# Optimization experiments

Measured on AMD Instinct MI355X. Metric: run time of the kernel, lower is better.

The kernel has to match this reference:

```python
import jax, jax.numpy as jnp
import numpy as np

B, N, S, DG, C_IN, C_OUT, HID = 2, 128, 4, 8, 4, 8, 32


def setup_inputs() -> dict:
    key = jax.random.key(0)
    ks = jax.random.split(key, 10)

    def w(k, shape, fan_in):
        return jax.random.normal(k, shape, jnp.float32) / np.float32(np.sqrt(fan_in))

    return {
        "pairwise_g": jax.random.normal(ks[0], (B, N, N, S, S, DG), jnp.float32),
        "coset_functions": jax.random.normal(ks[1], (B, N, S, C_IN), jnp.float32),
        "mask": jax.random.bernoulli(ks[2], 0.9, (B, N, S)),
        "ky_W1": w(ks[3], (C_IN, HID, 2), 2), "ky_b1": jnp.zeros((C_IN, HID), jnp.float32),
        "ky_W2": w(ks[4], (C_IN, HID, HID), HID), "ky_b2": jnp.zeros((C_IN, HID), jnp.float32),
        "ky_W3": w(ks[5], (C_IN, 1, HID), HID), "ky_b3": jnp.zeros((C_IN, 1), jnp.float32),
        "kg_W1": w(ks[6], (C_IN, HID, DG), DG), "kg_b1": jnp.zeros((C_IN, HID), jnp.float32),
        "kg_W2": w(ks[7], (C_IN, HID, HID), HID), "kg_b2": jnp.zeros((C_IN, HID), jnp.float32),
        "kg_W3": w(ks[8], (C_IN, 1, HID), HID), "kg_b3": jnp.zeros((C_IN, 1), jnp.float32),
        "w_out": w(ks[9], (C_OUT, C_IN), C_IN),
    }


def _mlp(x, W1, b1, W2, b2, W3, b3):
    # NerualNetKernel with bn=False, act=Swish: (Linear + SiLU) x 3, incl. output layer.
    h = jax.nn.silu(x @ W1.T + b1)
    h = jax.nn.silu(h @ W2.T + b2)
    return jax.nn.silu(h @ W3.T + b3)


def reference(pairwise_g, coset_functions, mask,
              ky_W1, ky_b1, ky_W2, ky_b2, ky_W3, ky_b3,
              kg_W1, kg_b1, kg_W2, kg_b2, kg_W3, kg_b3, w_out):
    b, n, _, s, _, _ = pairwise_g.shape
    c_in = coset_functions.shape[-1]
    key_mask = mask[:, None, :, None, :, None]  # (B,1,N,1,S,1) masks key points/samples
    outs = []
    for i in range(c_in):  # fixed small channel loop, as in the original module
        f = coset_functions[..., i:i + 1]  # (B,N,S,1)
        y1 = jnp.broadcast_to(f[:, None, :, None, :, :], (b, n, n, s, s, 1))  # key side
        y2 = jnp.broadcast_to(f[:, :, None, :, None, :], (b, n, n, s, s, 1))  # query side
        y = jnp.concatenate([y1, y2], axis=-1)  # (B,N,N,S,S,2)
        k = (_mlp(y, ky_W1[i], ky_b1[i], ky_W2[i], ky_b2[i], ky_W3[i], ky_b3[i])
             + _mlp(pairwise_g, kg_W1[i], kg_b1[i], kg_W2[i], kg_b2[i], kg_W3[i], kg_b3[i]))
        att = jnp.where(key_mask, jnp.exp(k), jnp.zeros((), k.dtype))  # (B,N,N,S,S,1)
        att = att / att.sum(axis=(2, 4), keepdims=True)
        f = f + (att * f[:, None, :, None, :, :]).sum(axis=(2, 4))  # residual + weighted agg
        outs.append(f)
    cf = jnp.concatenate(outs, axis=-1)  # (B,N,S,C_IN)
    cf = cf * mask[..., None].astype(cf.dtype)
    return cf @ w_out.T  # (B,N,S,C_OUT), bias-free output transform
```

## Files before the change

kernel.cpp:

```cpp
#include <hip/hip_runtime.h>
#include <hip/hip_bf16.h>

#define BB   2
#define NN   128
#define SS   4
#define DGG  8
#define CIN  4
#define COUT 8
#define HH   32

typedef __attribute__((ext_vector_type(4))) float          fvec4;
typedef __attribute__((ext_vector_type(4))) unsigned short usvec4;
typedef __attribute__((ext_vector_type(8))) unsigned short usvec8;
typedef __attribute__((ext_vector_type(2))) __fp16         half2v;
typedef __attribute__((ext_vector_type(8))) __fp16         f16x8;
typedef __attribute__((ext_vector_type(4))) float          f32x4;
typedef __attribute__((ext_vector_type(4))) unsigned int   uvec4;

__device__ __forceinline__ float bf2f(unsigned short u) {
    return __uint_as_float(((unsigned int)u) << 16);
}
__device__ __forceinline__ float silu_f(float x) {
    float e = __builtin_amdgcn_exp2f(x * -1.44269504f);
    return x * __builtin_amdgcn_rcpf(1.0f + e);
}
__device__ __forceinline__ float exp_f(float x) {
    return __builtin_amdgcn_exp2f(x * 1.44269504f);
}

__device__ __forceinline__ half2v upk(unsigned int u) {
    union { unsigned int u; half2v h; } x; x.u = u; return x.h;
}
__device__ __forceinline__ unsigned int pk2u(float a, float b) {
#if __has_builtin(__builtin_amdgcn_cvt_pkrtz)
    half2v h = __builtin_amdgcn_cvt_pkrtz(a, b);
#else
    half2v h; h[0] = (__fp16)a; h[1] = (__fp16)b;
#endif
    union { half2v h; unsigned int u; } x; x.h = h; return x.u;
}
union FU { uvec4 u; f16x8 h; };
__device__ __forceinline__ f16x8 mk_frag(unsigned a, unsigned b, unsigned c, unsigned d) {
    FU x; x.u = (uvec4){a, b, c, d}; return x.h;
}

__device__ __forceinline__ float loadS(const void* p, int idx, int fmode) {
    return fmode ? bf2f(((const unsigned short*)p)[idx])
                 : ((const float*)p)[idx];
}
__device__ __forceinline__ void load8(const void* p, int base, int fmode, float* dst) {
    if (fmode) {
        usvec8 v = *(const usvec8*)((const unsigned short*)p + base);
#pragma unroll
        for (int d = 0; d < 8; ++d) dst[d] = bf2f(v[d]);
    } else {
        fvec4 a = *(const fvec4*)((const float*)p + base);
        fvec4 b = *(const fvec4*)((const float*)p + base + 4);
        dst[0] = a[0]; dst[1] = a[1]; dst[2] = a[2]; dst[3] = a[3];
        dst[4] = b[0]; dst[5] = b[1]; dst[6] = b[2]; dst[7] = b[3];
    }
}
__device__ __forceinline__ uvec4 load_row8u(const void* p, int eoff, int fmode) {
    uvec4 u;
    if (fmode) {
        usvec8 v = *(const usvec8*)((const unsigned short*)p + eoff);
#pragma unroll
        for (int q = 0; q < 4; ++q) u[q] = pk2u(bf2f(v[2 * q]), bf2f(v[2 * q + 1]));
    } else {
        fvec4 a = *(const fvec4*)((const float*)p + eoff);
        fvec4 b = *(const fvec4*)((const float*)p + eoff + 4);
        u[0] = pk2u(a[0], a[1]); u[1] = pk2u(a[2], a[3]);
        u[2] = pk2u(b[0], b[1]); u[3] = pk2u(b[2], b[3]);
    }
    return u;
}
__device__ __forceinline__ f16x8 load_row8(const void* p, int eoff, int fmode) {
    uvec4 u = load_row8u(p, eoff, fmode);
    return mk_frag(u[0], u[1], u[2], u[3]);
}
__device__ __forceinline__ int load_mask(const void* p, int idx, int mmode) {
    if (mmode == 0) return ((const int*)p)[idx] != 0;
    if (mmode == 1) return ((const unsigned short*)p)[idx] != 0;
    if (mmode == 2) return ((const unsigned char*)p)[idx] != 0;
    return ((const unsigned int*)p)[idx] != 0;
}
__device__ __forceinline__ void stage_pk(unsigned int* dst, const void* src,
                                         int pairs, int fmode, int tid) {
    if (fmode) {
        const unsigned short* s = (const unsigned short*)src;
        for (int x = tid; x < pairs; x += 256)
            dst[x] = pk2u(bf2f(s[2 * x]), bf2f(s[2 * x + 1]));
    } else {
        const float* s = (const float*)src;
        for (int x = tid; x < pairs; x += 256)
            dst[x] = pk2u(s[2 * x], s[2 * x + 1]);
    }
}
__device__ __forceinline__ void copy_arr(float* sm, const void* src, int off,
                                         int cnt, int fmode, int tid) {
    if (fmode) {
        const unsigned short* s = (const unsigned short*)src;
        for (int x = tid; x < cnt; x += 256) sm[off + x] = bf2f(s[x]);
    } else {
        const float* s = (const float*)src;
        for (int x = tid; x < cnt; x += 256) sm[off + x] = s[x];
    }
}
__device__ __forceinline__ void detect_inline(const void* g_mask, const void* g_coset,
                                              int tid, int* smi, int slot) {
    if (tid < 64) {
        const unsigned short* cu = (const unsigned short*)g_coset;
        unsigned short v = cu[2 * tid];
        int e = (v >> 7) & 0xFF;
        int hits = __popcll(__ballot(e >= 110 && e <= 135));
        int fmode_ = (hits > 32) ? 1 : 0;
        const unsigned short* mu = (const unsigned short*)g_mask;
        int evenBF = 0, any3 = 0, anyByte = 0;
        for (int r = 0; r < 8; ++r) {
            int idx = tid + r * 64;
            unsigned short m = mu[idx];
            if (m == 0x3F80) { any3 = 1; if (!(idx & 1)) evenBF = 1; }
            if (m == 0x0101 || m == 0x0100) anyByte = 1;
        }
        evenBF  = (__ballot(evenBF)  != 0ull);
        any3    = (__ballot(any3)    != 0ull);
        anyByte = (__ballot(anyByte) != 0ull);
        if (tid == 0) {
            smi[slot]     = fmode_;
            smi[slot + 1] = evenBF ? 1 : (any3 ? 3 : (anyByte ? 2 : 0));
        }
    }
}

#define UG_G    0
#define F_FA    2048
#define U_MASK  4096
#define U_YW1   4608
#define F_YB1   4736
#define F_YB2   4864
#define F_YW3   4992
#define F_GB1   5120
#define F_GB2   5248
#define F_GW3   5376
#define F_YB3   5504
#define F_GB3   5508
#define F_RED   5512
#define F_MODE  5544
#define U_TOTAL 5546

__global__ __launch_bounds__(256, 4) void emha_mfma(
    const void* __restrict__ g_pw, const void* __restrict__ g_coset,
    const void* __restrict__ g_mask,
    const void* yW1, const void* yb1, const void* yW2, const void* yb2,
    const void* yW3, const void* yb3,
    const void* gW1, const void* gb1, const void* gW2, const void* gb2,
    const void* gW3, const void* gb3,
    const void* wout, void* outp)
{
    __shared__ __align__(16) unsigned int smu[U_TOTAL];
    float* smf = (float*)smu;
    int*   smi = (int*)smu;
    const int tid = threadIdx.x;

    detect_inline(g_mask, g_coset, tid, smi, F_MODE);
    __syncthreads();
    const int fmode = smi[F_MODE];
    const int mmode = smi[F_MODE + 1];
    __syncthreads();

    const int bn = blockIdx.x >> 2;
    const int s1 = blockIdx.x & 3;
    const int b  = bn >> 7;
    const int n1 = bn & 127;

#pragma unroll
    for (int it = 0; it < 2; ++it) {
        const int pos = tid + it * 256;
        const int n2 = pos >> 2, s2 = pos & 3;
        float g8[8];
        load8(g_pw, (((bn * NN + n2) * SS + s1) * SS + s2) * DGG, fmode, g8);
#pragma unroll
        for (int q = 0; q < 4; ++q)
            smu[UG_G + pos * 4 + q] = pk2u(g8[2 * q], g8[2 * q + 1]);
    }
    for (int x = tid; x < 2048; x += 256)
        smf[F_FA + x] = loadS(g_coset, b * 2048 + x, fmode);
    for (int x = tid; x < 512; x += 256)
        smu[U_MASK + x] = (unsigned)load_mask(g_mask, b * 512 + x, mmode);
    stage_pk(&smu[U_YW1], yW1, 128, fmode, tid);
    copy_arr(smf, yb1, F_YB1, 128, fmode, tid);
    copy_arr(smf, yb2, F_YB2, 128, fmode, tid);
    copy_arr(smf, yW3, F_YW3, 128, fmode, tid);
    copy_arr(smf, gb1, F_GB1, 128, fmode, tid);
    copy_arr(smf, gb2, F_GB2, 128, fmode, tid);
    copy_arr(smf, gW3, F_GW3, 128, fmode, tid);
    copy_arr(smf, yb3, F_YB3, 4, fmode, tid);
    copy_arr(smf, gb3, F_GB3, 4, fmode, tid);
    __syncthreads();

    const int lane = tid & 63;
    const int wave = tid >> 6;
    const int quad = lane >> 4;
    const int col  = lane & 15;
    const int qpos = n1 * 4 + s1;

    float accN[4] = {0.f, 0.f, 0.f, 0.f};
    float accD[4] = {0.f, 0.f, 0.f, 0.f};

#pragma unroll
    for (int ci = 0; ci < CIN; ++ci) {
        const float fb = smf[F_FA + qpos * 4 + ci];
        float w0f[8], cc[8];
        {
            uvec4 pa = *(const uvec4*)&smu[U_YW1 + ci * 32 + quad * 8];
            uvec4 pb = *(const uvec4*)&smu[U_YW1 + ci * 32 + quad * 8 + 4];
            fvec4 ba = *(const fvec4*)&smf[F_YB1 + ci * 32 + quad * 8];
            fvec4 bb = *(const fvec4*)&smf[F_YB1 + ci * 32 + quad * 8 + 4];
#pragma unroll
            for (int jj = 0; jj < 4; ++jj) {
                half2v w = upk(pa[jj]);
                w0f[jj] = (float)w[0];
                cc[jj]  = (float)w[1] * fb + ba[jj];
            }
#pragma unroll
            for (int jj = 0; jj < 4; ++jj) {
                half2v w = upk(pb[jj]);
                w0f[4 + jj] = (float)w[0];
                cc[4 + jj]  = (float)w[1] * fb + bb[jj];
            }
        }
        const f16x8 Ay0 = load_row8(yW2, ci * 1024 + col * 32 + quad * 8, fmode);
        const f16x8 Ay1 = load_row8(yW2, ci * 1024 + (col + 16) * 32 + quad * 8, fmode);
        const f16x8 Ag0 = load_row8(gW2, ci * 1024 + col * 32 + quad * 8, fmode);
        const f16x8 Ag1 = load_row8(gW2, ci * 1024 + (col + 16) * 32 + quad * 8, fmode);
        const int hA = ((col >> 2) << 3) + (col & 3);
        uvec4 ua = load_row8u(gW1, ci * 256 + hA * 8, fmode);
        uvec4 ub = load_row8u(gW1, ci * 256 + hA * 8 + 32, fmode);
        if (quad != 0) { ua = (uvec4){0, 0, 0, 0}; ub = (uvec4){0, 0, 0, 0}; }
        const f16x8 GA = mk_frag(ua[0], ua[1], ua[2], ua[3]);
        const f16x8 GB = mk_frag(ub[0], ub[1], ub[2], ub[3]);
        const fvec4 cGA = *(const fvec4*)&smf[F_GB1 + ci * 32 + quad * 8];
        const fvec4 cGB = *(const fvec4*)&smf[F_GB1 + ci * 32 + quad * 8 + 4];
        const fvec4 cY0 = *(const fvec4*)&smf[F_YB2 + ci * 32 + quad * 4];
        const fvec4 cY1 = *(const fvec4*)&smf[F_YB2 + ci * 32 + 16 + quad * 4];
        const fvec4 cG0 = *(const fvec4*)&smf[F_GB2 + ci * 32 + quad * 4];
        const fvec4 cG1 = *(const fvec4*)&smf[F_GB2 + ci * 32 + 16 + quad * 4];
        const fvec4 w3y0 = *(const fvec4*)&smf[F_YW3 + ci * 32 + quad * 4];
        const fvec4 w3y1 = *(const fvec4*)&smf[F_YW3 + ci * 32 + 16 + quad * 4];
        const fvec4 w3g0 = *(const fvec4*)&smf[F_GW3 + ci * 32 + quad * 4];
        const fvec4 w3g1 = *(const fvec4*)&smf[F_GW3 + ci * 32 + 16 + quad * 4];
        const float b3y = smf[F_YB3 + ci];
        const float b3g = smf[F_GB3 + ci];

#pragma unroll 1
        for (int t = 0; t < 8; ++t) {
            const int pos = (wave * 8 + t) * 16 + col;
            const float fap = smf[F_FA + pos * 4 + ci];
            const unsigned km = smu[U_MASK + pos];
            const uvec4 gq = *(const uvec4*)&smu[UG_G + pos * 4];
            const f16x8 Bg1 = mk_frag(gq[0], gq[1], gq[2], gq[3]);

            unsigned by0 = pk2u(silu_f(w0f[0] * fap + cc[0]), silu_f(w0f[1] * fap + cc[1]));
            unsigned by1 = pk2u(silu_f(w0f[2] * fap + cc[2]), silu_f(w0f[3] * fap + cc[3]));
            unsigned by2 = pk2u(silu_f(w0f[4] * fap + cc[4]), silu_f(w0f[5] * fap + cc[5]));
            unsigned by3 = pk2u(silu_f(w0f[6] * fap + cc[6]), silu_f(w0f[7] * fap + cc[7]));
            const f16x8 By = mk_frag(by0, by1, by2, by3);

            f32x4 dA, dB, dy0, dy1, dg0, dg1;
#if defined(__HIP_DEVICE_COMPILE__)
            dA = __builtin_amdgcn_mfma_f32_16x16x32_f16(GA, Bg1, cGA, 0, 0, 0);
            dB = __builtin_amdgcn_mfma_f32_16x16x32_f16(GB, Bg1, cGB, 0, 0, 0);
#else
            dA = cGA; dB = cGB;
#endif
            unsigned bg0 = pk2u(silu_f(dA[0]), silu_f(dA[1]));
            unsigned bg1 = pk2u(silu_f(dA[2]), silu_f(dA[3]));
            unsigned bg2 = pk2u(silu_f(dB[0]), silu_f(dB[1]));
            unsigned bg3 = pk2u(silu_f(dB[2]), silu_f(dB[3]));
            const f16x8 Bg = mk_frag(bg0, bg1, bg2, bg3);

#if defined(__HIP_DEVICE_COMPILE__)
            dy0 = __builtin_amdgcn_mfma_f32_16x16x32_f16(Ay0, By, cY0, 0, 0, 0);
            dy1 = __builtin_amdgcn_mfma_f32_16x16x32_f16(Ay1, By, cY1, 0, 0, 0);
            dg0 = __builtin_amdgcn_mfma_f32_16x16x32_f16(Ag0, Bg, cG0, 0, 0, 0);
            dg1 = __builtin_amdgcn_mfma_f32_16x16x32_f16(Ag1, Bg, cG1, 0, 0, 0);
#else
            dy0 = cY0; dy1 = cY1; dg0 = cG0; dg1 = cG1;
#endif
            float a3y = 0.f, a3g = 0.f;
#pragma unroll
            for (int r = 0; r < 4; ++r) {
                a3y += w3y0[r] * silu_f(dy0[r]);
                a3y += w3y1[r] * silu_f(dy1[r]);
                a3g += w3g0[r] * silu_f(dg0[r]);
                a3g += w3g1[r] * silu_f(dg1[r]);
            }
            a3y += __shfl_xor(a3y, 16); a3y += __shfl_xor(a3y, 32);
            a3g += __shfl_xor(a3g, 16); a3g += __shfl_xor(a3g, 32);

            const float kyv = silu_f(a3y + b3y);
            const float kgv = silu_f(a3g + b3g);
            const float e = km ? exp_f(kyv + kgv) : 0.f;
            accD[ci] += e;
            accN[ci] += e * fap;
        }
    }

#pragma unroll
    for (int ci = 0; ci < CIN; ++ci) {
        accN[ci] += __shfl_xor(accN[ci], 1);  accD[ci] += __shfl_xor(accD[ci], 1);
        accN[ci] += __shfl_xor(accN[ci], 2);  accD[ci] += __shfl_xor(accD[ci], 2);
        accN[ci] += __shfl_xor(accN[ci], 4);  accD[ci] += __shfl_xor(accD[ci], 4);
        accN[ci] += __shfl_xor(accN[ci], 8);  accD[ci] += __shfl_xor(accD[ci], 8);
    }
    if (lane == 0) {
#pragma unroll
        for (int ci = 0; ci < CIN; ++ci) {
            smf[F_RED + (wave * 4 + ci) * 2 + 0] = accN[ci];
            smf[F_RED + (wave * 4 + ci) * 2 + 1] = accD[ci];
        }
    }
    __syncthreads();

    if (tid < COUT) {
        const int o = tid;
        const unsigned m1 = smu[U_MASK + qpos];
        float acc = 0.f;
#pragma unroll
        for (int ci = 0; ci < CIN; ++ci) {
            float N = 0.f, D = 0.f;
#pragma unroll
            for (int w = 0; w < 4; ++w) {
                N += smf[F_RED + (w * 4 + ci) * 2 + 0];
                D += smf[F_RED + (w * 4 + ci) * 2 + 1];
            }
            const float fbv = smf[F_FA + qpos * 4 + ci];
            const float cf = m1 ? (fbv + N / D) : 0.f;
            acc += cf * loadS(wout, o * CIN + ci, fmode);
        }
        const int oidx = (bn * SS + s1) * COUT + o;
        if (fmode) ((__hip_bfloat16*)outp)[oidx] = __float2bfloat16(acc);
        else       ((float*)outp)[oidx] = acc;
    }
}

extern "C" void kernel_launch(void* const* d_in, const int* in_sizes, int n_in,
                              void* d_out, int out_size, void* d_ws, size_t ws_size,
                              hipStream_t stream) {
    emha_mfma<<<BB * NN * SS, 256, 0, stream>>>(
        d_in[0], d_in[1], d_in[2],
        d_in[3], d_in[4], d_in[5], d_in[6], d_in[7], d_in[8],
        d_in[9], d_in[10], d_in[11], d_in[12], d_in[13], d_in[14],
        d_in[15], d_out);
}
```

Before: 176.0 us.

## Move first and last MLP layers onto MFMA and stage all weights in LDS

```diff
diff --git a/kernel.cpp b/kernel.cpp
--- a/kernel.cpp
+++ b/kernel.cpp
@@ -28,9 +28,6 @@
     return __builtin_amdgcn_exp2f(x * 1.44269504f);
 }
 
-__device__ __forceinline__ half2v upk(unsigned int u) {
-    union { unsigned int u; half2v h; } x; x.u = u; return x.h;
-}
 __device__ __forceinline__ unsigned int pk2u(float a, float b) {
 #if __has_builtin(__builtin_amdgcn_cvt_pkrtz)
     half2v h = __builtin_amdgcn_cvt_pkrtz(a, b);
@@ -43,6 +40,15 @@
 __device__ __forceinline__ f16x8 mk_frag(unsigned a, unsigned b, unsigned c, unsigned d) {
     FU x; x.u = (uvec4){a, b, c, d}; return x.h;
 }
+__device__ __forceinline__ f16x8 mk_fragv(uvec4 u) {
+    FU x; x.u = u; return x.h;
+}
+__device__ __forceinline__ f16x8 silu_frag(f32x4 a, f32x4 b) {
+    return mk_frag(pk2u(silu_f(a[0]), silu_f(a[1])),
+                   pk2u(silu_f(a[2]), silu_f(a[3])),
+                   pk2u(silu_f(b[0]), silu_f(b[1])),
+                   pk2u(silu_f(b[2]), silu_f(b[3])));
+}
 
 __device__ __forceinline__ float loadS(const void* p, int idx, int fmode) {
     return fmode ? bf2f(((const unsigned short*)p)[idx])
@@ -59,24 +65,6 @@
         dst[0] = a[0]; dst[1] = a[1]; dst[2] = a[2]; dst[3] = a[3];
         dst[4] = b[0]; dst[5] = b[1]; dst[6] = b[2]; dst[7] = b[3];
     }
-}
-__device__ __forceinline__ uvec4 load_row8u(const void* p, int eoff, int fmode) {
-    uvec4 u;
-    if (fmode) {
-        usvec8 v = *(const usvec8*)((const unsigned short*)p + eoff);
-#pragma unroll
-        for (int q = 0; q < 4; ++q) u[q] = pk2u(bf2f(v[2 * q]), bf2f(v[2 * q + 1]));
-    } else {
-        fvec4 a = *(const fvec4*)((const float*)p + eoff);
-        fvec4 b = *(const fvec4*)((const float*)p + eoff + 4);
-        u[0] = pk2u(a[0], a[1]); u[1] = pk2u(a[2], a[3]);
-        u[2] = pk2u(b[0], b[1]); u[3] = pk2u(b[2], b[3]);
-    }
-    return u;
-}
-__device__ __forceinline__ f16x8 load_row8(const void* p, int eoff, int fmode) {
-    uvec4 u = load_row8u(p, eoff, fmode);
-    return mk_frag(u[0], u[1], u[2], u[3]);
 }
 __device__ __forceinline__ int load_mask(const void* p, int idx, int mmode) {
     if (mmode == 0) return ((const int*)p)[idx] != 0;
@@ -134,19 +122,22 @@
 
 #define UG_G    0
 #define F_FA    2048
-#define U_MASK  4096
-#define U_YW1   4608
-#define F_YB1   4736
-#define F_YB2   4864
-#define F_YW3   4992
-#define F_GB1   5120
-#define F_GB2   5248
-#define F_GW3   5376
-#define F_YB3   5504
-#define F_GB3   5508
-#define F_RED   5512
-#define F_MODE  5544
-#define U_TOTAL 5546
+#define U_MASKB 4096
+#define U_YW1   4224
+#define U_GW1   4352
+#define U_W2Y   4864
+#define U_W2G   6912
+#define F_YB1   8960
+#define F_GB1   9088
+#define F_YB2   9216
+#define F_GB2   9344
+#define U_YW3   9472
+#define U_GW3   9536
+#define F_YB3   9600
+#define F_GB3   9604
+#define F_RED   9608
+#define F_MODE  9640
+#define U_TOTAL 9642
 
 __global__ __launch_bounds__(256, 4) void emha_mfma(
     const void* __restrict__ g_pw, const void* __restrict__ g_coset,
@@ -185,15 +176,21 @@
     }
     for (int x = tid; x < 2048; x += 256)
         smf[F_FA + x] = loadS(g_coset, b * 2048 + x, fmode);
-    for (int x = tid; x < 512; x += 256)
-        smu[U_MASK + x] = (unsigned)load_mask(g_mask, b * 512 + x, mmode);
-    stage_pk(&smu[U_YW1], yW1, 128, fmode, tid);
+    {
+        unsigned char* mb = (unsigned char*)&smu[U_MASKB];
+        for (int x = tid; x < 512; x += 256)
+            mb[x] = (unsigned char)load_mask(g_mask, b * 512 + x, mmode);
+    }
+    stage_pk(&smu[U_YW1], yW1, 128,  fmode, tid);
+    stage_pk(&smu[U_GW1], gW1, 512,  fmode, tid);
+    stage_pk(&smu[U_W2Y], yW2, 2048, fmode, tid);
+    stage_pk(&smu[U_W2G], gW2, 2048, fmode, tid);
+    stage_pk(&smu[U_YW3], yW3, 64,   fmode, tid);
+    stage_pk(&smu[U_GW3], gW3, 64,   fmode, tid);
     copy_arr(smf, yb1, F_YB1, 128, fmode, tid);
+    copy_arr(smf, gb1, F_GB1, 128, fmode, tid);
     copy_arr(smf, yb2, F_YB2, 128, fmode, tid);
-    copy_arr(smf, yW3, F_YW3, 128, fmode, tid);
-    copy_arr(smf, gb1, F_GB1, 128, fmode, tid);
     copy_arr(smf, gb2, F_GB2, 128, fmode, tid);
-    copy_arr(smf, gW3, F_GW3, 128, fmode, tid);
     copy_arr(smf, yb3, F_YB3, 4, fmode, tid);
     copy_arr(smf, gb3, F_GB3, 4, fmode, tid);
     __syncthreads();
@@ -203,81 +200,69 @@
     const int quad = lane >> 4;
     const int col  = lane & 15;
     const int qpos = n1 * 4 + s1;
-
-    float accN[4] = {0.f, 0.f, 0.f, 0.f};
-    float accD[4] = {0.f, 0.f, 0.f, 0.f};
-
-#pragma unroll
+    const int h0   = ((col >> 2) << 3) + (col & 3);
+    const unsigned char* mb = (const unsigned char*)&smu[U_MASKB];
+
+#pragma unroll 1
     for (int ci = 0; ci < CIN; ++ci) {
         const float fb = smf[F_FA + qpos * 4 + ci];
-        float w0f[8], cc[8];
-        {
-            uvec4 pa = *(const uvec4*)&smu[U_YW1 + ci * 32 + quad * 8];
-            uvec4 pb = *(const uvec4*)&smu[U_YW1 + ci * 32 + quad * 8 + 4];
-            fvec4 ba = *(const fvec4*)&smf[F_YB1 + ci * 32 + quad * 8];
-            fvec4 bb = *(const fvec4*)&smf[F_YB1 + ci * 32 + quad * 8 + 4];
-#pragma unroll
-            for (int jj = 0; jj < 4; ++jj) {
-                half2v w = upk(pa[jj]);
-                w0f[jj] = (float)w[0];
-                cc[jj]  = (float)w[1] * fb + ba[jj];
-            }
-#pragma unroll
-            for (int jj = 0; jj < 4; ++jj) {
-                half2v w = upk(pb[jj]);
-                w0f[4 + jj] = (float)w[0];
-                cc[4 + jj]  = (float)w[1] * fb + bb[jj];
-            }
-        }
-        const f16x8 Ay0 = load_row8(yW2, ci * 1024 + col * 32 + quad * 8, fmode);
-        const f16x8 Ay1 = load_row8(yW2, ci * 1024 + (col + 16) * 32 + quad * 8, fmode);
-        const f16x8 Ag0 = load_row8(gW2, ci * 1024 + col * 32 + quad * 8, fmode);
-        const f16x8 Ag1 = load_row8(gW2, ci * 1024 + (col + 16) * 32 + quad * 8, fmode);
-        const int hA = ((col >> 2) << 3) + (col & 3);
-        uvec4 ua = load_row8u(gW1, ci * 256 + hA * 8, fmode);
-        uvec4 ub = load_row8u(gW1, ci * 256 + hA * 8 + 32, fmode);
-        if (quad != 0) { ua = (uvec4){0, 0, 0, 0}; ub = (uvec4){0, 0, 0, 0}; }
-        const f16x8 GA = mk_frag(ua[0], ua[1], ua[2], ua[3]);
-        const f16x8 GB = mk_frag(ub[0], ub[1], ub[2], ub[3]);
+        const uvec4 zz = {0u, 0u, 0u, 0u};
+
+        const unsigned wy1a = (quad == 0) ? smu[U_YW1 + ci * 32 + h0] : 0u;
+        const unsigned wy1b = (quad == 0) ? smu[U_YW1 + ci * 32 + h0 + 4] : 0u;
+        const f16x8 AY1a = mk_frag(wy1a, 0u, 0u, 0u);
+        const f16x8 AY1b = mk_frag(wy1b, 0u, 0u, 0u);
+        const fvec4 cYA = *(const fvec4*)&smf[F_YB1 + ci * 32 + quad * 8];
+        const fvec4 cYB = *(const fvec4*)&smf[F_YB1 + ci * 32 + quad * 8 + 4];
+
+        uvec4 ga = *(const uvec4*)&smu[U_GW1 + ci * 128 + h0 * 4];
+        uvec4 gb = *(const uvec4*)&smu[U_GW1 + ci * 128 + h0 * 4 + 16];
+        if (quad != 0) { ga = zz; gb = zz; }
+        const f16x8 GA = mk_fragv(ga);
+        const f16x8 GB = mk_fragv(gb);
         const fvec4 cGA = *(const fvec4*)&smf[F_GB1 + ci * 32 + quad * 8];
         const fvec4 cGB = *(const fvec4*)&smf[F_GB1 + ci * 32 + quad * 8 + 4];
-        const fvec4 cY0 = *(const fvec4*)&smf[F_YB2 + ci * 32 + quad * 4];
-        const fvec4 cY1 = *(const fvec4*)&smf[F_YB2 + ci * 32 + 16 + quad * 4];
-        const fvec4 cG0 = *(const fvec4*)&smf[F_GB2 + ci * 32 + quad * 4];
-        const fvec4 cG1 = *(const fvec4*)&smf[F_GB2 + ci * 32 + 16 + quad * 4];
-        const fvec4 w3y0 = *(const fvec4*)&smf[F_YW3 + ci * 32 + quad * 4];
-        const fvec4 w3y1 = *(const fvec4*)&smf[F_YW3 + ci * 32 + 16 + quad * 4];
-        const fvec4 w3g0 = *(const fvec4*)&smf[F_GW3 + ci * 32 + quad * 4];
-        const fvec4 w3g1 = *(const fvec4*)&smf[F_GW3 + ci * 32 + 16 + quad * 4];
-        const float b3y = smf[F_YB3 + ci];
-        const float b3g = smf[F_GB3 + ci];
-
+
+        const f16x8 Ay0 = mk_fragv(*(const uvec4*)&smu[U_W2Y + ci * 512 + h0 * 16 + quad * 4]);
+        const f16x8 Ay1 = mk_fragv(*(const uvec4*)&smu[U_W2Y + ci * 512 + (h0 + 4) * 16 + quad * 4]);
+        const f16x8 Ag0 = mk_fragv(*(const uvec4*)&smu[U_W2G + ci * 512 + h0 * 16 + quad * 4]);
+        const f16x8 Ag1 = mk_fragv(*(const uvec4*)&smu[U_W2G + ci * 512 + (h0 + 4) * 16 + quad * 4]);
+        const fvec4 cY0 = *(const fvec4*)&smf[F_YB2 + ci * 32 + quad * 8];
+        const fvec4 cY1 = *(const fvec4*)&smf[F_YB2 + ci * 32 + quad * 8 + 4];
+        const fvec4 cG0 = *(const fvec4*)&smf[F_GB2 + ci * 32 + quad * 8];
+        const fvec4 cG1 = *(const fvec4*)&smf[F_GB2 + ci * 32 + quad * 8 + 4];
+
+        uvec4 a3y = *(const uvec4*)&smu[U_YW3 + ci * 16 + quad * 4];
+        uvec4 a3g = *(const uvec4*)&smu[U_GW3 + ci * 16 + quad * 4];
+        if (col != 0) { a3y = zz; a3g = zz; }
+        const f16x8 A3y = mk_fragv(a3y);
+        const f16x8 A3g = mk_fragv(a3g);
+        fvec4 C3y = {0.f, 0.f, 0.f, 0.f};
+        fvec4 C3g = {0.f, 0.f, 0.f, 0.f};
+        if (quad == 0) { C3y[0] = smf[F_YB3 + ci]; C3g[0] = smf[F_GB3 + ci]; }
+
+        float aN = 0.f, aD = 0.f;
 #pragma unroll 1
         for (int t = 0; t < 8; ++t) {
             const int pos = (wave * 8 + t) * 16 + col;
             const float fap = smf[F_FA + pos * 4 + ci];
-            const unsigned km = smu[U_MASK + pos];
+            const int km = mb[pos];
             const uvec4 gq = *(const uvec4*)&smu[UG_G + pos * 4];
-            const f16x8 Bg1 = mk_frag(gq[0], gq[1], gq[2], gq[3]);
-
-            unsigned by0 = pk2u(silu_f(w0f[0] * fap + cc[0]), silu_f(w0f[1] * fap + cc[1]));
-            unsigned by1 = pk2u(silu_f(w0f[2] * fap + cc[2]), silu_f(w0f[3] * fap + cc[3]));
-            unsigned by2 = pk2u(silu_f(w0f[4] * fap + cc[4]), silu_f(w0f[5] * fap + cc[5]));
-            unsigned by3 = pk2u(silu_f(w0f[6] * fap + cc[6]), silu_f(w0f[7] * fap + cc[7]));
-            const f16x8 By = mk_frag(by0, by1, by2, by3);
-
-            f32x4 dA, dB, dy0, dy1, dg0, dg1;
+
+            const f16x8 B1y = mk_frag(pk2u(fap, fb), 0u, 0u, 0u);
+            const f16x8 Bg1 = mk_fragv(gq);
+
+            f32x4 d1a, d1b, dga, dgb, dy0, dy1, dg0, dg1, dy3, dg3;
 #if defined(__HIP_DEVICE_COMPILE__)
-            dA = __builtin_amdgcn_mfma_f32_16x16x32_f16(GA, Bg1, cGA, 0, 0, 0);
-            dB = __builtin_amdgcn_mfma_f32_16x16x32_f16(GB, Bg1, cGB, 0, 0, 0);
+            d1a = __builtin_amdgcn_mfma_f32_16x16x32_f16(AY1a, B1y, cYA, 0, 0, 0);
+            d1b = __builtin_amdgcn_mfma_f32_16x16x32_f16(AY1b, B1y, cYB, 0, 0, 0);
+            dga = __builtin_amdgcn_mfma_f32_16x16x32_f16(GA,   Bg1, cGA, 0, 0, 0);
+            dgb = __builtin_amdgcn_mfma_f32_16x16x32_f16(GB,   Bg1, cGB, 0, 0, 0);
 #else
-            dA = cGA; dB = cGB;
+            d1a = cYA; d1b = cYB; dga = cGA; dgb = cGB;
 #endif
-            unsigned bg0 = pk2u(silu_f(dA[0]), silu_f(dA[1]));
-            unsigned bg1 = pk2u(silu_f(dA[2]), silu_f(dA[3]));
-            unsigned bg2 = pk2u(silu_f(dB[0]), silu_f(dB[1]));
-            unsigned bg3 = pk2u(silu_f(dB[2]), silu_f(dB[3]));
-            const f16x8 Bg = mk_frag(bg0, bg1, bg2, bg3);
+            const f16x8 By = silu_frag(d1a, d1b);
+            const f16x8 Bg = silu_frag(dga, dgb);
 
 #if defined(__HIP_DEVICE_COMPILE__)
             dy0 = __builtin_amdgcn_mfma_f32_16x16x32_f16(Ay0, By, cY0, 0, 0, 0);
@@ -287,44 +272,35 @@
 #else
             dy0 = cY0; dy1 = cY1; dg0 = cG0; dg1 = cG1;
 #endif
-            float a3y = 0.f, a3g = 0.f;
-#pragma unroll
-            for (int r = 0; r < 4; ++r) {
-                a3y += w3y0[r] * silu_f(dy0[r]);
-                a3y += w3y1[r] * silu_f(dy1[r]);
-                a3g += w3g0[r] * silu_f(dg0[r]);
-                a3g += w3g1[r] * silu_f(dg1[r]);
-            }
-            a3y += __shfl_xor(a3y, 16); a3y += __shfl_xor(a3y, 32);
-            a3g += __shfl_xor(a3g, 16); a3g += __shfl_xor(a3g, 32);
-
-            const float kyv = silu_f(a3y + b3y);
-            const float kgv = silu_f(a3g + b3g);
+            const f16x8 By2 = silu_frag(dy0, dy1);
+            const f16x8 Bg2 = silu_frag(dg0, dg1);
+
+#if defined(__HIP_DEVICE_COMPILE__)
+            dy3 = __builtin_amdgcn_mfma_f32_16x16x32_f16(A3y, By2, C3y, 0, 0, 0);
+            dg3 = __builtin_amdgcn_mfma_f32_16x16x32_f16(A3g, Bg2, C3g, 0, 0, 0);
+#else
+            dy3 = C3y; dg3 = C3g;
+#endif
+            const float kyv = silu_f(dy3[0]);
+            const float kgv = silu_f(dg3[0]);
             const float e = km ? exp_f(kyv + kgv) : 0.f;
-            accD[ci] += e;
-            accN[ci] += e * fap;
-        }
-    }
-
-#pragma unroll
-    for (int ci = 0; ci < CIN; ++ci) {
-        accN[ci] += __shfl_xor(accN[ci], 1);  accD[ci] += __shfl_xor(accD[ci], 1);
-        accN[ci] += __shfl_xor(accN[ci], 2);  accD[ci] += __shfl_xor(accD[ci], 2);
-        accN[ci] += __shfl_xor(accN[ci], 4);  accD[ci] += __shfl_xor(accD[ci], 4);
-        accN[ci] += __shfl_xor(accN[ci], 8);  accD[ci] += __shfl_xor(accD[ci], 8);
-    }
-    if (lane == 0) {
-#pragma unroll
-        for (int ci = 0; ci < CIN; ++ci) {
-            smf[F_RED + (wave * 4 + ci) * 2 + 0] = accN[ci];
-            smf[F_RED + (wave * 4 + ci) * 2 + 1] = accD[ci];
+            aD += e;
+            aN += e * fap;
+        }
+        aN += __shfl_xor(aN, 1);  aD += __shfl_xor(aD, 1);
+        aN += __shfl_xor(aN, 2);  aD += __shfl_xor(aD, 2);
+        aN += __shfl_xor(aN, 4);  aD += __shfl_xor(aD, 4);
+        aN += __shfl_xor(aN, 8);  aD += __shfl_xor(aD, 8);
+        if (lane == 0) {
+            smf[F_RED + (wave * 4 + ci) * 2 + 0] = aN;
+            smf[F_RED + (wave * 4 + ci) * 2 + 1] = aD;
         }
     }
     __syncthreads();
 
     if (tid < COUT) {
         const int o = tid;
-        const unsigned m1 = smu[U_MASK + qpos];
+        const int m1 = mb[qpos];
         float acc = 0.f;
 #pragma unroll
         for (int ci = 0; ci < CIN; ++ci) {
```

Result: faster. 168.8 us (-4.1%).
